# Performance work log

Measured on AMD Instinct MI355X. Metric: run time of the kernel, lower is better.

## Reference

```python
import jax, jax.numpy as jnp
import numpy as np

B, F, E, A, T, H = 16384, 1024, 28, 2, 128, 4
HD = T // H  # head dim = 32

def _ln(x, g, b, eps=1e-5):
    m = jnp.mean(x, axis=-1, keepdims=True)
    v = jnp.var(x, axis=-1, keepdims=True)
    return (x - m) / jnp.sqrt(v + eps) * g + b

def _gelu(x):
    return jax.nn.gelu(x, approximate=False)  # torch nn.GELU default (erf)

def setup_inputs() -> dict:
    key = jax.random.key(0)
    ks = iter(jax.random.split(key, 48))
    def rn(shape, s=0.02):
        return jax.random.normal(next(ks), shape, jnp.float32) * s
    d = dict(
        fusion_feat=jax.random.normal(next(ks), (B, F), jnp.float32),
        explicit_logits=jax.random.normal(next(ks), (B, E), jnp.float32),
        implicit_logits=jax.random.normal(next(ks), (B, E), jnp.float32),
        affect_vec=jax.random.normal(next(ks), (B, A), jnp.float32),
        ln_exp_g=jnp.ones((E,), jnp.float32), ln_exp_b=jnp.zeros((E,), jnp.float32),
        W_exp=rn((E, T)), b_exp=jnp.zeros((T,), jnp.float32),
        ln_imp_g=jnp.ones((E,), jnp.float32), ln_imp_b=jnp.zeros((E,), jnp.float32),
        W_imp=rn((E, T)), b_imp=jnp.zeros((T,), jnp.float32),
        ln_aff_g=jnp.ones((A,), jnp.float32), ln_aff_b=jnp.zeros((A,), jnp.float32),
        W_aff=rn((A, T)), b_aff=jnp.zeros((T,), jnp.float32),
        Wq_in=rn((F, T)), bq_in=jnp.zeros((T,), jnp.float32),   # query_proj
        Wq=rn((T, T)), bq=jnp.zeros((T,), jnp.float32),         # MHA in_proj q
        Wk=rn((T, T)), bk=jnp.zeros((T,), jnp.float32),         # MHA in_proj k
        Wv=rn((T, T)), bv=jnp.zeros((T,), jnp.float32),         # MHA in_proj v
        Wo=rn((T, T)), bo=jnp.zeros((T,), jnp.float32),         # MHA out_proj
        Wc=rn((T, F)), bc=jnp.zeros((F,), jnp.float32),         # context_proj
        Ws=rn((3 * T, F)), bs=jnp.zeros((F,), jnp.float32),     # summary_proj
        Wg1=rn((2 * F, F)), bg1=jnp.zeros((F,), jnp.float32),   # gate layer 1
        Wg2=rn((F, F)), bg2=jnp.zeros((F,), jnp.float32),       # gate layer 2
        ln_out_g=jnp.ones((F,), jnp.float32), ln_out_b=jnp.zeros((F,), jnp.float32),
    )
    return d

def reference(fusion_feat, explicit_logits, implicit_logits, affect_vec,
              ln_exp_g, ln_exp_b, W_exp, b_exp,
              ln_imp_g, ln_imp_b, W_imp, b_imp,
              ln_aff_g, ln_aff_b, W_aff, b_aff,
              Wq_in, bq_in, Wq, bq, Wk, bk, Wv, bv, Wo, bo,
              Wc, bc, Ws, bs, Wg1, bg1, Wg2, bg2, ln_out_g, ln_out_b):
    p_exp = jax.nn.softmax(explicit_logits, axis=-1)
    p_imp = jax.nn.softmax(implicit_logits, axis=-1)
    exp_e = _gelu(_ln(p_exp, ln_exp_g, ln_exp_b) @ W_exp + b_exp)       # (B,T)
    imp_e = _gelu(_ln(p_imp, ln_imp_g, ln_imp_b) @ W_imp + b_imp)       # (B,T)
    aff_e = _gelu(_ln(affect_vec, ln_aff_g, ln_aff_b) @ W_aff + b_aff)  # (B,T)
    tokens = jnp.stack([exp_e, imp_e, aff_e], axis=1)                   # (B,3,T)
    q = fusion_feat @ Wq_in + bq_in                                     # (B,T)
    # tiny 1-query x 3-key multi-head cross attention (dropout=eval/identity)
    qh = (q @ Wq + bq).reshape(B, H, HD)
    kh = (tokens @ Wk + bk).reshape(B, 3, H, HD)
    vh = (tokens @ Wv + bv).reshape(B, 3, H, HD)
    scores = jnp.einsum('bhd,bshd->bhs', qh, kh) / np.float32(np.sqrt(HD))
    w = jax.nn.softmax(scores, axis=-1)                                 # (B,H,3)
    attn_weights = jnp.mean(w, axis=1)                                  # avg heads -> (B,3)
    attn_out = jnp.einsum('bhs,bshd->bhd', w, vh).reshape(B, T) @ Wo + bo
    context = attn_out @ Wc + bc                                        # (B,F)
    gate_h = _gelu(jnp.concatenate([fusion_feat, context], axis=-1) @ Wg1 + bg1)
    gate = jax.nn.sigmoid(gate_h @ Wg2 + bg2)
    refined = _ln(fusion_feat + gate * context, ln_out_g, ln_out_b)
    summary = _gelu(jnp.concatenate([exp_e, imp_e, aff_e], axis=-1) @ Ws + bs)
    return refined, attn_weights, summary
```

## Files before the change

kernel.cpp:

```cpp
#include <hip/hip_runtime.h>
#include <hip/hip_bf16.h>
#include <stdint.h>


using bf16 = __hip_bfloat16;
typedef __bf16 bf16x8 __attribute__((ext_vector_type(8)));
typedef float f32x4 __attribute__((ext_vector_type(4)));

__device__ __forceinline__ float b2f(bf16 x) { return __bfloat162float(x); }
__device__ __forceinline__ bf16 f2b(float x) { return __float2bfloat16(x); }

__device__ __forceinline__ float fast_tanh(float y) {
  float z = fabsf(y);
  float t = __expf(-2.f * z);
  float r = (1.f - t) / (1.f + t);
  return copysignf(r, y);
}
__device__ __forceinline__ float gelu_f(float x) {
  return 0.5f * x * (1.f + fast_tanh(0.7978845608028654f * (x + 0.044715f * x * x * x)));
}
__device__ __forceinline__ float sigmoid_f(float v) {
  return 1.f / (1.f + __expf(-v));
}

__device__ __forceinline__ void async_ld16(const void* g, void* l) {
  using GP = const __attribute__((address_space(1))) uint32_t*;
  using LP = __attribute__((address_space(3))) uint32_t*;
  __builtin_amdgcn_global_load_lds((GP)g, (LP)l, 16, 0, 0);
}

__global__ void ffb_convert(const float* __restrict__ src, bf16* __restrict__ dst) {
  size_t i = ((size_t)blockIdx.x * 256 + threadIdx.x) * 4;
  float4 v = *reinterpret_cast<const float4*>(src + i);
  ushort4 o;
  o.x = __builtin_bit_cast(unsigned short, f2b(v.x));
  o.y = __builtin_bit_cast(unsigned short, f2b(v.y));
  o.z = __builtin_bit_cast(unsigned short, f2b(v.z));
  o.w = __builtin_bit_cast(unsigned short, f2b(v.w));
  *reinterpret_cast<ushort4*>(dst + i) = o;
}

template <int EPI, typename OutT, int MT>
__launch_bounds__(256)
__global__ void gemm128(const bf16* A0, const bf16* A1, int ksplit, int lda0, int lda1,
                        const bf16* __restrict__ BT, int K,
                        const float* __restrict__ bias,
                        OutT* out, int ldo,
                        const bf16* ffp, const bf16* ctxp, int ldfc)
{
  constexpr int MIC = MT / 32;
  __shared__ uint16_t smA[MT * 64];
  __shared__ uint16_t smB[128 * 64];
  const int tid = threadIdx.x;
  const int w = tid >> 6;
  const int l = tid & 63;
  const int m0 = blockIdx.x * MT;
  const int n0 = blockIdx.y * 128;
  const int wr = w >> 1, wc = w & 1;
  const int lrow = l & 15, lquad = l >> 4;
  const int rb = w * 8 + (l >> 3);
  const int cpos = l & 7;

  const f32x4 vzero = {0.f, 0.f, 0.f, 0.f};
  f32x4 acc[MIC][4];
#pragma unroll
  for (int i = 0; i < MIC; i++)
#pragma unroll
    for (int j = 0; j < 4; j++) acc[i][j] = vzero;

  for (int k0 = 0; k0 < K; k0 += 64) {
    __syncthreads();
#pragma unroll
    for (int i = 0; i < MIC; i++) {
      int row = i * 32 + rb;
      int cg = cpos ^ (row & 7);
      int kcol = k0 + cg * 8;
      const bf16* gp = (kcol < ksplit)
                           ? (A0 + (size_t)(m0 + row) * lda0 + kcol)
                           : (A1 + (size_t)(m0 + row) * lda1 + (kcol - ksplit));
      async_ld16(gp, &smA[(i * 32 + w * 8) * 64]);
    }
#pragma unroll
    for (int i = 0; i < 4; i++) {
      int row = i * 32 + rb;
      int cg = cpos ^ (row & 7);
      const bf16* gq = BT + (size_t)(n0 + row) * K + k0 + cg * 8;
      async_ld16(gq, &smB[(i * 32 + w * 8) * 64]);
    }
    __syncthreads();
#pragma unroll
    for (int kk = 0; kk < 2; kk++) {
      bf16x8 af[MIC], bfr[4];
      const int cc = kk * 4 + lquad;
#pragma unroll
      for (int mi = 0; mi < MIC; mi++) {
        int r = wr * (MT / 2) + mi * 16 + lrow;
        af[mi] = *(const bf16x8*)&smA[r * 64 + ((cc ^ (r & 7)) << 3)];
      }
#pragma unroll
      for (int ni = 0; ni < 4; ni++) {
        int r = wc * 64 + ni * 16 + lrow;
        bfr[ni] = *(const bf16x8*)&smB[r * 64 + ((cc ^ (r & 7)) << 3)];
      }
#pragma unroll
      for (int mi = 0; mi < MIC; mi++)
#pragma unroll
        for (int ni = 0; ni < 4; ni++)
          acc[mi][ni] =
              __builtin_amdgcn_mfma_f32_16x16x32_bf16(af[mi], bfr[ni], acc[mi][ni], 0, 0, 0);
    }
  }

#pragma unroll
  for (int mi = 0; mi < MIC; mi++) {
#pragma unroll
    for (int ni = 0; ni < 4; ni++) {
#pragma unroll
      for (int r = 0; r < 4; r++) {
        int row = m0 + wr * (MT / 2) + mi * 16 + lquad * 4 + r;
        int col = n0 + wc * 64 + ni * 16 + lrow;
        float v = acc[mi][ni][r] + (bias ? bias[col] : 0.f);
        if (EPI == 1) v = gelu_f(v);
        if (EPI == 2) {
          float gate = sigmoid_f(v);
          size_t fo = (size_t)row * ldfc + col;
          v = b2f(ffp[fo]) + gate * b2f(ctxp[fo]);
        }
        if constexpr (__is_same(OutT, float))
          out[(size_t)row * ldo + col] = v;
        else
          out[(size_t)row * ldo + col] = f2b(v);
      }
    }
  }
}

template <int EPI, typename OutT>
__launch_bounds__(512, 2)
__global__ void gemm256(const bf16* A0, const bf16* A1, int ksplit, int lda0, int lda1,
                        const bf16* __restrict__ BT, int K,
                        const float* __restrict__ bias,
                        OutT* out, int ldo,
                        const bf16* ffp, const bf16* ctxp, int ldfc)
{
  __shared__ uint16_t smA[2][256 * 64];
  __shared__ uint16_t smB[2][256 * 64];
  const int tid = threadIdx.x;
  const int w = tid >> 6;
  const int l = tid & 63;
  const int m0 = blockIdx.x * 256;
  const int n0 = blockIdx.y * 256;
  const int wr = w >> 2;
  const int wc = w & 3;
  const int lrow = l & 15, lquad = l >> 4;
  const int rb = tid >> 3;
  const int cpos = tid & 7;
  const int NT = K >> 6;

  const f32x4 vzero = {0.f, 0.f, 0.f, 0.f};
  f32x4 acc[8][4];
#pragma unroll
  for (int mi = 0; mi < 8; mi++)
#pragma unroll
    for (int ni = 0; ni < 4; ni++) acc[mi][ni] = vzero;

  auto stage = [&](int buf, int tt) {
    const int k0 = tt << 6;
    const bf16* Ab; int la, kc;
    if (k0 < ksplit) { Ab = A0; la = lda0; kc = k0; }
    else             { Ab = A1; la = lda1; kc = k0 - ksplit; }
#pragma unroll
    for (int i = 0; i < 4; i++) {
      const int row = i * 64 + rb;
      const int cg = cpos ^ (row & 7);
      async_ld16(Ab + (size_t)(m0 + row) * la + kc + cg * 8,
                 &smA[buf][(i * 64 + w * 8) * 64]);
    }
#pragma unroll
    for (int i = 0; i < 4; i++) {
      const int row = i * 64 + rb;
      const int cg = cpos ^ (row & 7);
      async_ld16(BT + (size_t)(n0 + row) * K + k0 + cg * 8,
                 &smB[buf][(i * 64 + w * 8) * 64]);
    }
  };

  int cur = 0;

  auto readfrags = [&](int kk, bf16x8 (&af)[8], bf16x8 (&bfr)[4]) {
    const int cc = kk * 4 + lquad;
#pragma unroll
    for (int mi = 0; mi < 8; mi++) {
      int r = wr * 128 + mi * 16 + lrow;
      af[mi] = *(const bf16x8*)&smA[cur][r * 64 + (((cc) ^ (r & 7)) << 3)];
    }
#pragma unroll
    for (int ni = 0; ni < 4; ni++) {
      int r = wc * 64 + ni * 16 + lrow;
      bfr[ni] = *(const bf16x8*)&smB[cur][r * 64 + (((cc) ^ (r & 7)) << 3)];
    }
  };
  auto domfma = [&](bf16x8 (&af)[8], bf16x8 (&bfr)[4]) {
#pragma unroll
    for (int mi = 0; mi < 8; mi++)
#pragma unroll
      for (int ni = 0; ni < 4; ni++)
        acc[mi][ni] =
            __builtin_amdgcn_mfma_f32_16x16x32_bf16(af[mi], bfr[ni], acc[mi][ni], 0, 0, 0);
  };

  stage(0, 0);
  stage(1, 1);
  asm volatile("s_waitcnt vmcnt(8)" ::: "memory");
  __builtin_amdgcn_s_barrier();
  __builtin_amdgcn_sched_barrier(0);

  for (int t = 0; t < NT; ++t) {
    bf16x8 af[8], bfr[4];
    readfrags(0, af, bfr);
    __builtin_amdgcn_s_setprio(1);
    domfma(af, bfr);
    __builtin_amdgcn_s_setprio(0);
    readfrags(1, af, bfr);
    asm volatile("s_waitcnt lgkmcnt(0)" ::: "memory");
    __builtin_amdgcn_s_barrier();
    __builtin_amdgcn_sched_barrier(0);
    if (t + 2 < NT) stage(cur, t + 2);
    __builtin_amdgcn_s_setprio(1);
    domfma(af, bfr);
    __builtin_amdgcn_s_setprio(0);
    if (t + 2 < NT) {
      asm volatile("s_waitcnt vmcnt(8)" ::: "memory");
    } else {
      asm volatile("s_waitcnt vmcnt(0)" ::: "memory");
    }
    __builtin_amdgcn_s_barrier();
    __builtin_amdgcn_sched_barrier(0);
    cur ^= 1;
  }

#pragma unroll
  for (int mi = 0; mi < 8; mi++) {
#pragma unroll
    for (int ni = 0; ni < 4; ni++) {
#pragma unroll
      for (int r = 0; r < 4; r++) {
        int row = m0 + wr * 128 + mi * 16 + lquad * 4 + r;
        int col = n0 + wc * 64 + ni * 16 + lrow;
        float v = acc[mi][ni][r] + (bias ? bias[col] : 0.f);
        if (EPI == 1) v = gelu_f(v);
        if (EPI == 2) {
          float gate = sigmoid_f(v);
          size_t fo = (size_t)row * ldfc + col;
          v = b2f(ffp[fo]) + gate * b2f(ctxp[fo]);
        }
        if constexpr (__is_same(OutT, float))
          out[(size_t)row * ldo + col] = v;
        else
          out[(size_t)row * ldo + col] = f2b(v);
      }
    }
  }
}

__global__ void transpose_cvt(const float* __restrict__ in, bf16* __restrict__ out,
                              int R, int C)
{
  __shared__ float tile[32][33];
  const int tx = threadIdx.x & 31, ty = threadIdx.x >> 5;
  const int c0 = blockIdx.x * 32, r0 = blockIdx.y * 32;
#pragma unroll
  for (int i = 0; i < 4; i++) {
    int r = ty + i * 8;
    tile[r][tx] = in[(size_t)(r0 + r) * C + c0 + tx];
  }
  __syncthreads();
#pragma unroll
  for (int i = 0; i < 4; i++) {
    int c = ty + i * 8;
    out[(size_t)(c0 + c) * R + r0 + tx] = f2b(tile[tx][c]);
  }
}

__global__ void prep_small(
    const float* __restrict__ Wk, const float* __restrict__ bk,
    const float* __restrict__ Wv, const float* __restrict__ bv,
    const float* __restrict__ Wq_in, const float* __restrict__ bq_in,
    const float* __restrict__ Wq, const float* __restrict__ bq,
    const float* __restrict__ Wo, const float* __restrict__ bo,
    const float* __restrict__ Wc, const float* __restrict__ bc,
    bf16* WKVT, float* BKV, float* BQQ, float* BOC, bf16* WQINB, bf16* WOB)
{
  int idx = blockIdx.x * 256 + threadIdx.x;
  if (idx < 32768) {
    int n = idx >> 7, k = idx & 127;
    WKVT[idx] = f2b((n < 128) ? Wk[k * 128 + n] : Wv[k * 128 + (n - 128)]);
    return;
  }
  idx -= 32768;
  if (idx < 256) { BKV[idx] = (idx < 128) ? bk[idx] : bv[idx - 128]; return; }
  idx -= 256;
  if (idx < 128) {
    float s = bq[idx];
    for (int u = 0; u < 128; u++) s += bq_in[u] * Wq[u * 128 + idx];
    BQQ[idx] = s;
    return;
  }
  idx -= 128;
  if (idx < 1024) {
    float s = bc[idx];
    for (int t = 0; t < 128; t++) s += bo[t] * Wc[t * 1024 + idx];
    BOC[idx] = s;
    return;
  }
  idx -= 1024;
  if (idx < 131072) { WQINB[idx] = f2b(Wq_in[idx]); return; }
  idx -= 131072;
  if (idx < 16384) { WOB[idx] = f2b(Wo[idx]); return; }
}

__device__ __forceinline__ void emb28(const float* __restrict__ logits,
                                      const float* __restrict__ g,
                                      const float* __restrict__ bb,
                                      const float* __restrict__ W,
                                      const float* __restrict__ wb,
                                      bf16* __restrict__ out, int t,
                                      float* sv, float* sp)
{
  if (t < 28) sv[t] = logits[t];
  __syncthreads();
  float mx = sv[0];
#pragma unroll
  for (int e = 1; e < 28; e++) mx = fmaxf(mx, sv[e]);
  if (t < 28) sp[t] = __expf(sv[t] - mx);
  __syncthreads();
  float sum = 0.f;
#pragma unroll
  for (int e = 0; e < 28; e++) sum += sp[e];
  float inv = 1.f / sum;
  float sp2 = 0.f;
#pragma unroll
  for (int e = 0; e < 28; e++) { float p = sp[e] * inv; sp2 += p * p; }
  const float mean = 1.f / 28.f;
  float var = sp2 * (1.f / 28.f) - mean * mean;
  float rstd = rsqrtf(var + 1e-5f);
  __syncthreads();
  if (t < 28) sp[t] = (sp[t] * inv - mean) * rstd * g[t] + bb[t];
  __syncthreads();
  float acc = wb[t];
#pragma unroll
  for (int e = 0; e < 28; e++) acc += sp[e] * W[e * 128 + t];
  out[t] = f2b(gelu_f(acc));
  __syncthreads();
}

__global__ void tokens_kernel(
    const float* __restrict__ exl, const float* __restrict__ iml, const float* __restrict__ affv,
    const float* __restrict__ geg, const float* __restrict__ geb,
    const float* __restrict__ Wex, const float* __restrict__ bex,
    const float* __restrict__ gig, const float* __restrict__ gib,
    const float* __restrict__ Wim, const float* __restrict__ bim,
    const float* __restrict__ gag, const float* __restrict__ gab,
    const float* __restrict__ Waf, const float* __restrict__ baf,
    bf16* __restrict__ tokens)
{
  __shared__ float sv[28], sp[28];
  const int b = blockIdx.x, t = threadIdx.x;
  bf16* trow = tokens + (size_t)b * 384;
  emb28(exl + (size_t)b * 28, geg, geb, Wex, bex, trow, t, sv, sp);
  emb28(iml + (size_t)b * 28, gig, gib, Wim, bim, trow + 128, t, sv, sp);
  float a0 = affv[(size_t)b * 2 + 0];
  float a1 = affv[(size_t)b * 2 + 1];
  float m = 0.5f * (a0 + a1);
  float d0 = a0 - m, d1 = a1 - m;
  float var = 0.5f * (d0 * d0 + d1 * d1);
  float rstd = rsqrtf(var + 1e-5f);
  float l0 = d0 * rstd * gag[0] + gab[0];
  float l1 = d1 * rstd * gag[1] + gab[1];
  float acc = baf[t] + l0 * Waf[t] + l1 * Waf[128 + t];
  trow[256 + t] = f2b(gelu_f(acc));
}

__global__ void attn_kernel(const bf16* __restrict__ qh, const bf16* __restrict__ kvh,
                            bf16* __restrict__ apre, float* __restrict__ attw)
{
  const int b = blockIdx.x, t = threadIdx.x;
  float q = b2f(qh[(size_t)b * 128 + t]);
  const bf16* kv = kvh + (size_t)b * 3 * 256;
  float s[3], v[3];
#pragma unroll
  for (int i = 0; i < 3; i++) {
    float k = b2f(kv[i * 256 + t]);
    v[i] = b2f(kv[i * 256 + 128 + t]);
    float r = q * k;
#pragma unroll
    for (int off = 16; off > 0; off >>= 1) r += __shfl_down(r, off, 32);
    r = __shfl(r, 0, 32);
    s[i] = r * 0.17677669529663687f;
  }
  float mx = fmaxf(s[0], fmaxf(s[1], s[2]));
  float e0 = __expf(s[0] - mx), e1 = __expf(s[1] - mx), e2 = __expf(s[2] - mx);
  float inv = 1.f / (e0 + e1 + e2);
  float w0 = e0 * inv, w1 = e1 * inv, w2 = e2 * inv;
  apre[(size_t)b * 128 + t] = f2b(w0 * v[0] + w1 * v[1] + w2 * v[2]);
  __shared__ float aw[4][3];
  if ((t & 31) == 0) { int h = t >> 5; aw[h][0] = w0; aw[h][1] = w1; aw[h][2] = w2; }
  __syncthreads();
  if (t < 3)
    attw[(size_t)b * 3 + t] = 0.25f * (aw[0][t] + aw[1][t] + aw[2][t] + aw[3][t]);
}

__global__ void ln_out_kernel(const bf16* __restrict__ x, const float* __restrict__ g,
                              const float* __restrict__ bb, float* __restrict__ out)
{
  const int row = blockIdx.x, t = threadIdx.x;
  const bf16* xr = x + (size_t)row * 1024;
  ushort4 u = *reinterpret_cast<const ushort4*>(xr + t * 4);
  float v0 = __uint_as_float((uint32_t)u.x << 16);
  float v1 = __uint_as_float((uint32_t)u.y << 16);
  float v2 = __uint_as_float((uint32_t)u.z << 16);
  float v3 = __uint_as_float((uint32_t)u.w << 16);
  float s = v0 + v1 + v2 + v3;
  float s2 = v0 * v0 + v1 * v1 + v2 * v2 + v3 * v3;
#pragma unroll
  for (int off = 32; off > 0; off >>= 1) {
    s += __shfl_down(s, off, 64);
    s2 += __shfl_down(s2, off, 64);
  }
  __shared__ float ls[4], ls2[4];
  const int w = t >> 6;
  if ((t & 63) == 0) { ls[w] = s; ls2[w] = s2; }
  __syncthreads();
  float S = ls[0] + ls[1] + ls[2] + ls[3];
  float S2 = ls2[0] + ls2[1] + ls2[2] + ls2[3];
  float mean = S * (1.f / 1024.f);
  float var = S2 * (1.f / 1024.f) - mean * mean;
  float rstd = rsqrtf(var + 1e-5f);
  const int c = t * 4;
  float4 o;
  o.x = (v0 - mean) * rstd * g[c + 0] + bb[c + 0];
  o.y = (v1 - mean) * rstd * g[c + 1] + bb[c + 1];
  o.z = (v2 - mean) * rstd * g[c + 2] + bb[c + 2];
  o.w = (v3 - mean) * rstd * g[c + 3] + bb[c + 3];
  *reinterpret_cast<float4*>(out + (size_t)row * 1024 + c) = o;
}

extern "C" void kernel_launch(void* const* d_in, const int* in_sizes, int n_in,
                              void* d_out, int out_size, void* d_ws, size_t ws_size,
                              hipStream_t stream)
{
  const float* ff   = (const float*)d_in[0];
  const float* exl  = (const float*)d_in[1];
  const float* iml  = (const float*)d_in[2];
  const float* affv = (const float*)d_in[3];
  const float* geg = (const float*)d_in[4],  *geb = (const float*)d_in[5];
  const float* Wex = (const float*)d_in[6],  *bex = (const float*)d_in[7];
  const float* gig = (const float*)d_in[8],  *gib = (const float*)d_in[9];
  const float* Wim = (const float*)d_in[10], *bim = (const float*)d_in[11];
  const float* gag = (const float*)d_in[12], *gab = (const float*)d_in[13];
  const float* Waf = (const float*)d_in[14], *baf = (const float*)d_in[15];
  const float* Wq_in = (const float*)d_in[16], *bq_in = (const float*)d_in[17];
  const float* Wq = (const float*)d_in[18], *bq = (const float*)d_in[19];
  const float* Wk = (const float*)d_in[20], *bk = (const float*)d_in[21];
  const float* Wv = (const float*)d_in[22], *bv = (const float*)d_in[23];
  const float* Wo = (const float*)d_in[24], *bo = (const float*)d_in[25];
  const float* Wc = (const float*)d_in[26], *bc = (const float*)d_in[27];
  const float* Ws = (const float*)d_in[28], *bs = (const float*)d_in[29];
  const float* Wg1 = (const float*)d_in[30], *bg1 = (const float*)d_in[31];
  const float* Wg2 = (const float*)d_in[32], *bg2 = (const float*)d_in[33];
  const float* lng = (const float*)d_in[34], *lnb = (const float*)d_in[35];

  char* ws = (char*)d_ws;
  bf16*  WKVT = (bf16*)(ws + 0);
  float* BKV  = (float*)(ws + 65536);
  bf16*  WQQT = (bf16*)(ws + 66560);
  float* BQQ  = (float*)(ws + 328704);
  bf16*  WOCT = (bf16*)(ws + 329216);
  float* BOC  = (float*)(ws + 591360);
  bf16*  WST  = (bf16*)(ws + 595456);
  bf16*  WG1T = (bf16*)(ws + 1381888);
  bf16*  WG2T = (bf16*)(ws + 5576192);
  bf16*  FFB  = (bf16*)(ws + 7673344);
  bf16*  PRE  = (bf16*)(ws + 7673344);
  bf16*  TOK  = (bf16*)(ws + 41227776);
  bf16*  QH   = (bf16*)(ws + 53810688);
  bf16*  APRE = (bf16*)(ws + 58004992);

  bf16* WQT   = (bf16*)(ws + 53810688);
  bf16* WOB   = (bf16*)(ws + 53810688 + 32768);
  bf16* WQINB = (bf16*)(ws + 53810688 + 65536);
  bf16* WCT   = (bf16*)(ws + 53810688 + 327680);

  float* outp = (float*)d_out;
  float* out_refined = outp;
  float* out_attw    = outp + 16777216;
  float* out_summary = outp + 16826368;
  bf16* CTX   = (bf16*)out_refined;
  bf16* KVH   = (bf16*)out_summary;
  bf16* GATEH = (bf16*)out_summary;

  ffb_convert<<<16384, 256, 0, stream>>>(ff, FFB);
  prep_small<<<710, 256, 0, stream>>>(Wk, bk, Wv, bv, Wq_in, bq_in, Wq, bq,
                                      Wo, bo, Wc, bc, WKVT, BKV, BQQ, BOC, WQINB, WOB);
  transpose_cvt<<<dim3(4, 4),   256, 0, stream>>>(Wq,  WQT,  128, 128);
  transpose_cvt<<<dim3(32, 4),  256, 0, stream>>>(Wc,  WCT,  128, 1024);
  transpose_cvt<<<dim3(32, 12), 256, 0, stream>>>(Ws,  WST,  384, 1024);
  transpose_cvt<<<dim3(32, 64), 256, 0, stream>>>(Wg1, WG1T, 2048, 1024);
  transpose_cvt<<<dim3(32, 32), 256, 0, stream>>>(Wg2, WG2T, 1024, 1024);
  gemm128<0, bf16, 128><<<dim3(1, 8), 256, 0, stream>>>(WQT, WQT, 128, 128, 128, WQINB, 128,
                                                        nullptr, WQQT, 1024, nullptr, nullptr, 0);
  gemm128<0, bf16, 128><<<dim3(8, 1), 256, 0, stream>>>(WCT, WCT, 128, 128, 128, WOB, 128,
                                                        nullptr, WOCT, 128, nullptr, nullptr, 0);
  tokens_kernel<<<16384, 128, 0, stream>>>(exl, iml, affv, geg, geb, Wex, bex,
                                           gig, gib, Wim, bim, gag, gab, Waf, baf, TOK);
  gemm128<0, bf16, 64><<<dim3(256, 1), 256, 0, stream>>>(FFB, FFB, 1024, 1024, 1024, WQQT, 1024,
                                                         BQQ, QH, 128, nullptr, nullptr, 0);
  gemm128<0, bf16, 128><<<dim3(384, 2), 256, 0, stream>>>(TOK, TOK, 128, 128, 128, WKVT, 128,
                                                          BKV, KVH, 256, nullptr, nullptr, 0);
  attn_kernel<<<16384, 128, 0, stream>>>(QH, KVH, APRE, out_attw);
  gemm128<0, bf16, 128><<<dim3(128, 8), 256, 0, stream>>>(APRE, APRE, 128, 128, 128, WOCT, 128,
                                                          BOC, CTX, 1024, nullptr, nullptr, 0);
  gemm256<1, bf16><<<dim3(64, 4), 512, 0, stream>>>(FFB, CTX, 1024, 1024, 1024, WG1T, 2048,
                                                    bg1, GATEH, 1024, nullptr, nullptr, 0);
  gemm256<2, bf16><<<dim3(64, 4), 512, 0, stream>>>(GATEH, GATEH, 1024, 1024, 1024, WG2T, 1024,
                                                    bg2, PRE, 1024, FFB, CTX, 1024);
  gemm256<1, float><<<dim3(64, 4), 512, 0, stream>>>(TOK, TOK, 384, 384, 384, WST, 384,
                                                     bs, out_summary, 1024, nullptr, nullptr, 0);
  ln_out_kernel<<<16384, 256, 0, stream>>>(PRE, lng, lnb, out_refined);
}
```

Measured before the change: 604.7 us.

## Restructure gemm256 main loop into interleaved quarter-tile load/MFMA stages; merge transposes

The 256x256 GEMM main loop is split into eight sub-phases per pair of K tiles. Each phase reads a quarter of the A/B fragments, issues half-tile async global loads for a future stage, and runs a 4x2x2 MFMA block between barriers with raised priority. The goal is to overlap global loads and LDS reads with MFMA work at finer granularity than the old two-phase loop. The five weight-transpose launches are also merged into one kernel to cut launch overhead. The new schedule assumes NT is even (K a multiple of 128) and uses more barriers per K tile.

```diff
diff --git a/kernel.cpp b/kernel.cpp
--- a/kernel.cpp
+++ b/kernel.cpp
@@ -164,79 +164,122 @@
 #pragma unroll
     for (int ni = 0; ni < 4; ni++) acc[mi][ni] = vzero;
 
-  auto stage = [&](int buf, int tt) {
+  auto stageA = [&](int buf, int half, int tt) {
+    if (tt >= NT) return;
     const int k0 = tt << 6;
     const bf16* Ab; int la, kc;
     if (k0 < ksplit) { Ab = A0; la = lda0; kc = k0; }
     else             { Ab = A1; la = lda1; kc = k0 - ksplit; }
 #pragma unroll
-    for (int i = 0; i < 4; i++) {
-      const int row = i * 64 + rb;
+    for (int i = 0; i < 2; i++) {
+      const int row = half * 128 + i * 64 + rb;
       const int cg = cpos ^ (row & 7);
       async_ld16(Ab + (size_t)(m0 + row) * la + kc + cg * 8,
-                 &smA[buf][(i * 64 + w * 8) * 64]);
-    }
-#pragma unroll
-    for (int i = 0; i < 4; i++) {
-      const int row = i * 64 + rb;
+                 &smA[buf][(half * 128 + i * 64 + w * 8) * 64]);
+    }
+  };
+  auto stageB = [&](int buf, int half, int tt) {
+    if (tt >= NT) return;
+    const int k0 = tt << 6;
+#pragma unroll
+    for (int i = 0; i < 2; i++) {
+      const int row = half * 128 + i * 64 + rb;
       const int cg = cpos ^ (row & 7);
       async_ld16(BT + (size_t)(n0 + row) * K + k0 + cg * 8,
-                 &smB[buf][(i * 64 + w * 8) * 64]);
-    }
-  };
-
-  int cur = 0;
-
-  auto readfrags = [&](int kk, bf16x8 (&af)[8], bf16x8 (&bfr)[4]) {
-    const int cc = kk * 4 + lquad;
-#pragma unroll
-    for (int mi = 0; mi < 8; mi++) {
-      int r = wr * 128 + mi * 16 + lrow;
-      af[mi] = *(const bf16x8*)&smA[cur][r * 64 + (((cc) ^ (r & 7)) << 3)];
-    }
-#pragma unroll
-    for (int ni = 0; ni < 4; ni++) {
-      int r = wc * 64 + ni * 16 + lrow;
-      bfr[ni] = *(const bf16x8*)&smB[cur][r * 64 + (((cc) ^ (r & 7)) << 3)];
-    }
-  };
-  auto domfma = [&](bf16x8 (&af)[8], bf16x8 (&bfr)[4]) {
-#pragma unroll
-    for (int mi = 0; mi < 8; mi++)
-#pragma unroll
-      for (int ni = 0; ni < 4; ni++)
-        acc[mi][ni] =
-            __builtin_amdgcn_mfma_f32_16x16x32_bf16(af[mi], bfr[ni], acc[mi][ni], 0, 0, 0);
-  };
-
-  stage(0, 0);
-  stage(1, 1);
-  asm volatile("s_waitcnt vmcnt(8)" ::: "memory");
+                 &smB[buf][(half * 128 + i * 64 + w * 8) * 64]);
+    }
+  };
+
+  bf16x8 a[4][2], b0[2][2], b1[2][2];
+
+  auto rdA = [&](int buf, int miBlk) {
+#pragma unroll
+    for (int mi = 0; mi < 4; mi++)
+#pragma unroll
+      for (int kk = 0; kk < 2; kk++) {
+        int r = wr * 128 + miBlk * 64 + mi * 16 + lrow;
+        int cc = kk * 4 + lquad;
+        a[mi][kk] = *(const bf16x8*)&smA[buf][r * 64 + ((cc ^ (r & 7)) << 3)];
+      }
+  };
+  auto rdB0 = [&](int buf) {
+#pragma unroll
+    for (int ni = 0; ni < 2; ni++)
+#pragma unroll
+      for (int kk = 0; kk < 2; kk++) {
+        int r = wc * 64 + ni * 16 + lrow;
+        int cc = kk * 4 + lquad;
+        b0[ni][kk] = *(const bf16x8*)&smB[buf][r * 64 + ((cc ^ (r & 7)) << 3)];
+      }
+  };
+  auto rdB1 = [&](int buf) {
+#pragma unroll
+    for (int ni = 0; ni < 2; ni++)
+#pragma unroll
+      for (int kk = 0; kk < 2; kk++) {
+        int r = wc * 64 + 32 + ni * 16 + lrow;
+        int cc = kk * 4 + lquad;
+        b1[ni][kk] = *(const bf16x8*)&smB[buf][r * 64 + ((cc ^ (r & 7)) << 3)];
+      }
+  };
+  auto mm = [&](int miBlk, int niBlk, bf16x8 (&bf)[2][2]) {
+#pragma unroll
+    for (int mi = 0; mi < 4; mi++)
+#pragma unroll
+      for (int ni = 0; ni < 2; ni++)
+#pragma unroll
+        for (int kk = 0; kk < 2; kk++)
+          acc[miBlk * 4 + mi][niBlk * 2 + ni] = __builtin_amdgcn_mfma_f32_16x16x32_bf16(
+              a[mi][kk], bf[ni][kk], acc[miBlk * 4 + mi][niBlk * 2 + ni], 0, 0, 0);
+  };
+
+  auto fence_mid = [&]() {
+    __builtin_amdgcn_s_barrier();
+    asm volatile("s_waitcnt lgkmcnt(0)" ::: "memory");
+    __builtin_amdgcn_sched_barrier(0);
+    __builtin_amdgcn_s_setprio(1);
+  };
+  auto fence_end = [&](bool wait4) {
+    __builtin_amdgcn_s_setprio(0);
+    __builtin_amdgcn_sched_barrier(0);
+    if (wait4) asm volatile("s_waitcnt vmcnt(4)" ::: "memory");
+    __builtin_amdgcn_s_barrier();
+    __builtin_amdgcn_sched_barrier(0);
+  };
+
+  stageB(0, 0, 0); stageB(0, 1, 0); stageA(0, 0, 0); stageA(0, 1, 0);
+  stageB(1, 0, 1); stageB(1, 1, 1);
+  asm volatile("s_waitcnt vmcnt(4)" ::: "memory");
   __builtin_amdgcn_s_barrier();
   __builtin_amdgcn_sched_barrier(0);
 
-  for (int t = 0; t < NT; ++t) {
-    bf16x8 af[8], bfr[4];
-    readfrags(0, af, bfr);
-    __builtin_amdgcn_s_setprio(1);
-    domfma(af, bfr);
-    __builtin_amdgcn_s_setprio(0);
-    readfrags(1, af, bfr);
-    asm volatile("s_waitcnt lgkmcnt(0)" ::: "memory");
-    __builtin_amdgcn_s_barrier();
-    __builtin_amdgcn_sched_barrier(0);
-    if (t + 2 < NT) stage(cur, t + 2);
-    __builtin_amdgcn_s_setprio(1);
-    domfma(af, bfr);
-    __builtin_amdgcn_s_setprio(0);
-    if (t + 2 < NT) {
-      asm volatile("s_waitcnt vmcnt(8)" ::: "memory");
-    } else {
-      asm volatile("s_waitcnt vmcnt(0)" ::: "memory");
-    }
-    __builtin_amdgcn_s_barrier();
-    __builtin_amdgcn_sched_barrier(0);
-    cur ^= 1;
+  const int NI = NT >> 1;
+#pragma unroll 1
+  for (int t = 0; t < NI; ++t) {
+    const int To = 2 * t + 1;
+    const int Tn = 2 * t + 2;
+    rdA(0, 0); rdB0(0);
+    stageA(1, 0, To);
+    fence_mid(); mm(0, 0, b0); fence_end(false);
+    rdB1(0);
+    stageA(1, 1, To);
+    fence_mid(); mm(0, 1, b1); fence_end(false);
+    rdA(0, 1);
+    stageB(0, 0, Tn);
+    fence_mid(); mm(1, 1, b1); fence_end(false);
+    stageB(0, 1, Tn);
+    fence_mid(); mm(1, 0, b0); fence_end(true);
+    rdA(1, 0); rdB0(1);
+    stageA(0, 0, Tn);
+    fence_mid(); mm(0, 0, b0); fence_end(false);
+    rdB1(1);
+    stageA(0, 1, Tn);
+    fence_mid(); mm(0, 1, b1); fence_end(false);
+    rdA(1, 1);
+    stageB(1, 0, Tn + 1);
+    fence_mid(); mm(1, 1, b1); fence_end(false);
+    stageB(1, 1, Tn + 1);
+    fence_mid(); mm(1, 0, b0); fence_end(true);
   }
 
 #pragma unroll
@@ -263,12 +306,21 @@
   }
 }
 
-__global__ void transpose_cvt(const float* __restrict__ in, bf16* __restrict__ out,
-                              int R, int C)
+__global__ void transpose_all(const float* __restrict__ Wq, const float* __restrict__ Wc,
+                              const float* __restrict__ Ws, const float* __restrict__ Wg1,
+                              const float* __restrict__ Wg2,
+                              bf16* WQT, bf16* WCT, bf16* WST, bf16* WG1T, bf16* WG2T)
 {
   __shared__ float tile[32][33];
+  int bid = blockIdx.x;
+  const float* in; bf16* outp; int R, C, bx, by;
+  if (bid < 16)              { in = Wq;  outp = WQT;  R = 128;  C = 128;  bx = bid & 3;  by = bid >> 2; }
+  else if ((bid -= 16) < 128)  { in = Wc;  outp = WCT;  R = 128;  C = 1024; bx = bid & 31; by = bid >> 5; }
+  else if ((bid -= 128) < 384) { in = Ws;  outp = WST;  R = 384;  C = 1024; bx = bid & 31; by = bid >> 5; }
+  else if ((bid -= 384) < 2048){ in = Wg1; outp = WG1T; R = 2048; C = 1024; bx = bid & 31; by = bid >> 5; }
+  else { bid -= 2048;            in = Wg2; outp = WG2T; R = 1024; C = 1024; bx = bid & 31; by = bid >> 5; }
   const int tx = threadIdx.x & 31, ty = threadIdx.x >> 5;
-  const int c0 = blockIdx.x * 32, r0 = blockIdx.y * 32;
+  const int c0 = bx * 32, r0 = by * 32;
 #pragma unroll
   for (int i = 0; i < 4; i++) {
     int r = ty + i * 8;
@@ -278,7 +330,7 @@
 #pragma unroll
   for (int i = 0; i < 4; i++) {
     int c = ty + i * 8;
-    out[(size_t)(c0 + c) * R + r0 + tx] = f2b(tile[tx][c]);
+    outp[(size_t)(c0 + c) * R + r0 + tx] = f2b(tile[tx][c]);
   }
 }
 
@@ -502,11 +554,7 @@
   ffb_convert<<<16384, 256, 0, stream>>>(ff, FFB);
   prep_small<<<710, 256, 0, stream>>>(Wk, bk, Wv, bv, Wq_in, bq_in, Wq, bq,
                                       Wo, bo, Wc, bc, WKVT, BKV, BQQ, BOC, WQINB, WOB);
-  transpose_cvt<<<dim3(4, 4),   256, 0, stream>>>(Wq,  WQT,  128, 128);
-  transpose_cvt<<<dim3(32, 4),  256, 0, stream>>>(Wc,  WCT,  128, 1024);
-  transpose_cvt<<<dim3(32, 12), 256, 0, stream>>>(Ws,  WST,  384, 1024);
-  transpose_cvt<<<dim3(32, 64), 256, 0, stream>>>(Wg1, WG1T, 2048, 1024);
-  transpose_cvt<<<dim3(32, 32), 256, 0, stream>>>(Wg2, WG2T, 1024, 1024);
+  transpose_all<<<3600, 256, 0, stream>>>(Wq, Wc, Ws, Wg1, Wg2, WQT, WCT, WST, WG1T, WG2T);
   gemm128<0, bf16, 128><<<dim3(1, 8), 256, 0, stream>>>(WQT, WQT, 128, 128, 128, WQINB, 128,
                                                         nullptr, WQQT, 1024, nullptr, nullptr, 0);
   gemm128<0, bf16, 128><<<dim3(8, 1), 256, 0, stream>>>(WCT, WCT, 128, 128, 128, WOB, 128,
```

Result: faster. 592.1 us (-2.1%).
